# Kernel tuning notes

Measured on AMD Instinct MI355X. Metric: run time of the kernel, lower is better.

The kernel has to match this reference:

```python
import jax, jax.numpy as jnp
import numpy as np

IN_FEATURES = 1024
OUT_FEATURES = 1024
NUM_GRIDS = 8
GRID_MIN, GRID_MAX = -2.0, 2.0
DENOM = (GRID_MAX - GRID_MIN) / (NUM_GRIDS - 1)
LN_EPS = 1e-5
GRID = jnp.linspace(GRID_MIN, GRID_MAX, NUM_GRIDS)


def setup_inputs() -> dict:
    key = jax.random.key(0)
    k_x, k_sw, k_bw = jax.random.split(key, 3)
    N = 8192
    x = jax.random.normal(k_x, (N, IN_FEATURES), dtype=jnp.float32)
    ln_gamma = jnp.ones((IN_FEATURES,), dtype=jnp.float32)
    ln_beta = jnp.zeros((IN_FEATURES,), dtype=jnp.float32)
    # trunc_normal(std=0.1) approximated by scaled normal
    spline_w = 0.1 * jax.random.normal(k_sw, (OUT_FEATURES, IN_FEATURES * NUM_GRIDS), dtype=jnp.float32)
    base_w = jax.random.normal(k_bw, (OUT_FEATURES, IN_FEATURES), dtype=jnp.float32) * (1.0 / np.sqrt(IN_FEATURES))
    base_b = jnp.zeros((OUT_FEATURES,), dtype=jnp.float32)
    return {"x": x, "ln_gamma": ln_gamma, "ln_beta": ln_beta,
            "spline_w": spline_w, "base_w": base_w, "base_b": base_b}


def reference(x, ln_gamma, ln_beta, spline_w, base_w, base_b):
    # LayerNorm over last dim
    mu = jnp.mean(x, axis=-1, keepdims=True)
    var = jnp.var(x, axis=-1, keepdims=True)
    xn = (x - mu) * jax.lax.rsqrt(var + LN_EPS) * ln_gamma + ln_beta
    # RBF basis: [N, in, G]
    basis = jnp.exp(-jnp.square((xn[..., None] - GRID) / DENOM))
    basis = basis.reshape(x.shape[0], IN_FEATURES * NUM_GRIDS)
    y = jnp.einsum('nk,ok->no', basis, spline_w)
    y = y + jnp.einsum('nd,od->no', jax.nn.silu(x), base_w) + base_b
    return y
```

## Files before the change

kernel.cpp:

```cpp
#include <hip/hip_runtime.h>
#include <hip/hip_bf16.h>
#include <stdint.h>

#define IN_F 1024
#define OUT_F 1024
#define NG 8
#define KSPLINE 8192
#define KDIM 9216
#define M_ROWS 8192
#define LOG2E 1.4426950408889634f
#define DENOMV 0.5714285714285714f
#define INV_DENOM 1.75f

using bf16_t = __bf16;
using bf16x8 = __attribute__((ext_vector_type(8))) __bf16;
using f32x4  = __attribute__((ext_vector_type(4))) float;

#define AS1 __attribute__((address_space(1)))
#define AS3 __attribute__((address_space(3)))

__device__ inline unsigned short f2bf(float f) {
    unsigned int u = __float_as_uint(f);
    u += 0x7fffu + ((u >> 16) & 1u);
    return (unsigned short)(u >> 16);
}

__global__ __launch_bounds__(256) void prep_w_kernel(
        const float* __restrict__ sw, const float* __restrict__ bw,
        bf16_t* __restrict__ W) {
    int idx = blockIdx.x * 256 + threadIdx.x;
    int o   = idx / 2304;
    int k4  = idx - o * 2304;
    float4 v;
    if (k4 < 2048) v = ((const float4*)sw)[(size_t)o * 2048 + k4];
    else           v = ((const float4*)bw)[(size_t)o * 256 + (k4 - 2048)];
    unsigned int lo = (unsigned int)f2bf(v.x) | ((unsigned int)f2bf(v.y) << 16);
    unsigned int hi = (unsigned int)f2bf(v.z) | ((unsigned int)f2bf(v.w) << 16);
    ((uint2*)W)[idx] = make_uint2(lo, hi);
}

__global__ __launch_bounds__(256) void prep_a_kernel(
        const float* __restrict__ x, const float* __restrict__ gamma,
        const float* __restrict__ beta, bf16_t* __restrict__ A) {
    int row = blockIdx.x;
    int tid = threadIdx.x;
    const float4 xv = ((const float4*)(x + (size_t)row * IN_F))[tid];
    float s  = xv.x + xv.y + xv.z + xv.w;
    float s2 = xv.x * xv.x + xv.y * xv.y + xv.z * xv.z + xv.w * xv.w;
#pragma unroll
    for (int off = 32; off > 0; off >>= 1) {
        s  += __shfl_down(s, off);
        s2 += __shfl_down(s2, off);
    }
    __shared__ float red[8];
    int wave = tid >> 6, lane = tid & 63;
    if (lane == 0) { red[wave] = s; red[4 + wave] = s2; }
    __syncthreads();
    s  = red[0] + red[1] + red[2] + red[3];
    s2 = red[4] + red[5] + red[6] + red[7];
    float mu   = s * (1.0f / IN_F);
    float var  = s2 * (1.0f / IN_F) - mu * mu;
    float rstd = rsqrtf(var + 1e-5f);

    bf16_t* Arow = A + (size_t)row * KDIM;
    float xa[4] = {xv.x, xv.y, xv.z, xv.w};
    unsigned short silu_us[4];
#pragma unroll
    for (int j = 0; j < 4; ++j) {
        int f = tid * 4 + j;
        float xs = xa[j];
        float xn = (xs - mu) * rstd * gamma[f] + beta[f];
        unsigned int pk[4];
#pragma unroll
        for (int g = 0; g < 4; ++g) {
            float t0 = (xn - (-2.0f + (float)(2 * g)     * DENOMV)) * INV_DENOM;
            float t1 = (xn - (-2.0f + (float)(2 * g + 1) * DENOMV)) * INV_DENOM;
            float b0 = exp2f(t0 * t0 * -LOG2E);
            float b1 = exp2f(t1 * t1 * -LOG2E);
            pk[g] = (unsigned int)f2bf(b0) | ((unsigned int)f2bf(b1) << 16);
        }
        ((uint4*)(Arow + (size_t)f * NG))[0] = make_uint4(pk[0], pk[1], pk[2], pk[3]);
        float sg = xs / (1.0f + exp2f(-xs * LOG2E));
        silu_us[j] = f2bf(sg);
    }
    unsigned int slo = (unsigned int)silu_us[0] | ((unsigned int)silu_us[1] << 16);
    unsigned int shi = (unsigned int)silu_us[2] | ((unsigned int)silu_us[3] << 16);
    ((uint2*)(Arow + KSPLINE))[tid] = make_uint2(slo, shi);
}

__global__ __launch_bounds__(256, 2) void gemm_kernel(
        const bf16_t* __restrict__ A, const bf16_t* __restrict__ W,
        const float* __restrict__ bias, float* __restrict__ C) {
    __shared__ alignas(16) bf16_t As[128 * 32];
    __shared__ alignas(16) bf16_t Bs[128 * 32];
    const int bm = blockIdx.x, bn = blockIdx.y;
    const int tid = threadIdx.x;
    const int wave = tid >> 6, lane = tid & 63;
    const int wm = wave >> 1, wn = wave & 1;

    f32x4 acc[4][4] = {};

    const bf16_t* gAj[2];
    const bf16_t* gBj[2];
    int ldsOff[2];
#pragma unroll
    for (int j = 0; j < 2; ++j) {
        int chunk = wave * 128 + j * 64 + lane;
        int r  = chunk >> 2;
        int c8 = (chunk & 3) * 8;
        gAj[j] = A + (size_t)(bm * 128 + r) * KDIM + c8;
        gBj[j] = W + (size_t)(bn * 128 + r) * KDIM + c8;
        ldsOff[j] = chunk * 8;
    }

    const int lm = lane & 15;
    const int lk = (lane >> 4) * 8;

    for (int kt = 0; kt < KDIM / 32; ++kt) {
        __syncthreads();
#pragma unroll
        for (int j = 0; j < 2; ++j) {
            __builtin_amdgcn_global_load_lds(
                (const AS1 void*)(gAj[j] + kt * 32), (AS3 void*)(As + ldsOff[j]), 16, 0, 0);
            __builtin_amdgcn_global_load_lds(
                (const AS1 void*)(gBj[j] + kt * 32), (AS3 void*)(Bs + ldsOff[j]), 16, 0, 0);
        }
        __syncthreads();

        bf16x8 a[4], b[4];
#pragma unroll
        for (int i = 0; i < 4; ++i) {
            a[i] = *(const bf16x8*)(As + (wm * 64 + i * 16 + lm) * 32 + lk);
            b[i] = *(const bf16x8*)(Bs + (wn * 64 + i * 16 + lm) * 32 + lk);
        }
#pragma unroll
        for (int mi = 0; mi < 4; ++mi)
#pragma unroll
            for (int ni = 0; ni < 4; ++ni)
                acc[mi][ni] = __builtin_amdgcn_mfma_f32_16x16x32_bf16(
                    a[mi], b[ni], acc[mi][ni], 0, 0, 0);
    }

    const int cn = lane & 15;
    const int rm = (lane >> 4) * 4;
#pragma unroll
    for (int ni = 0; ni < 4; ++ni) {
        int col = bn * 128 + wn * 64 + ni * 16 + cn;
        float bv = bias[col];
#pragma unroll
        for (int mi = 0; mi < 4; ++mi) {
            int row = bm * 128 + wm * 64 + mi * 16 + rm;
            float* Cp = C + (size_t)row * OUT_F + col;
#pragma unroll
            for (int r = 0; r < 4; ++r)
                Cp[(size_t)r * OUT_F] = acc[mi][ni][r] + bv;
        }
    }
}

extern "C" void kernel_launch(void* const* d_in, const int* in_sizes, int n_in,
                              void* d_out, int out_size, void* d_ws, size_t ws_size,
                              hipStream_t stream) {
    const float* x     = (const float*)d_in[0];
    const float* gamma = (const float*)d_in[1];
    const float* beta  = (const float*)d_in[2];
    const float* sw    = (const float*)d_in[3];
    const float* bw    = (const float*)d_in[4];
    const float* bb    = (const float*)d_in[5];
    float* out = (float*)d_out;

    char* ws = (char*)d_ws;
    const size_t Wbytes = (size_t)OUT_F * KDIM * 2;
    bf16_t* Wb = (bf16_t*)ws;
    bf16_t* Ab = (bf16_t*)(ws + Wbytes);

    const size_t rowBytes = (size_t)KDIM * 2;
    size_t avail = ws_size > Wbytes ? ws_size - Wbytes : 0;
    int chunk = (int)(avail / rowBytes);
    chunk &= ~127;
    if (chunk > M_ROWS) chunk = M_ROWS;
    if (chunk < 128) chunk = 128;

    prep_w_kernel<<<(OUT_F * 2304) / 256, 256, 0, stream>>>(sw, bw, Wb);

    for (int r0 = 0; r0 < M_ROWS; r0 += chunk) {
        int rows = (M_ROWS - r0) < chunk ? (M_ROWS - r0) : chunk;
        prep_a_kernel<<<rows, 256, 0, stream>>>(x + (size_t)r0 * IN_F, gamma, beta, Ab);
        dim3 g(rows / 128, OUT_F / 128);
        gemm_kernel<<<g, dim3(256), 0, stream>>>(Ab, Wb, bb, out + (size_t)r0 * OUT_F);
    }
}
```

Measured before the change: 346.8 us.

## Split GEMM K dimension across two blocks with atomic accumulation

```diff
diff --git a/kernel.cpp b/kernel.cpp
--- a/kernel.cpp
+++ b/kernel.cpp
@@ -8,6 +8,8 @@
 #define KSPLINE 8192
 #define KDIM 9216
 #define M_ROWS 8192
+#define SPLITK 2
+#define KHALF (KDIM / SPLITK)
 #define LOG2E 1.4426950408889634f
 #define DENOMV 0.5714285714285714f
 #define INV_DENOM 1.75f
@@ -44,9 +46,12 @@
         const float* __restrict__ beta, bf16_t* __restrict__ A) {
     int row = blockIdx.x;
     int tid = threadIdx.x;
-    const float4 xv = ((const float4*)(x + (size_t)row * IN_F))[tid];
-    float s  = xv.x + xv.y + xv.z + xv.w;
-    float s2 = xv.x * xv.x + xv.y * xv.y + xv.z * xv.z + xv.w * xv.w;
+    const float* xr = x + (size_t)row * IN_F;
+    float xv[4];
+#pragma unroll
+    for (int j = 0; j < 4; ++j) xv[j] = xr[j * 256 + tid];
+    float s  = xv[0] + xv[1] + xv[2] + xv[3];
+    float s2 = xv[0]*xv[0] + xv[1]*xv[1] + xv[2]*xv[2] + xv[3]*xv[3];
 #pragma unroll
     for (int off = 32; off > 0; off >>= 1) {
         s  += __shfl_down(s, off);
@@ -63,12 +68,12 @@
     float rstd = rsqrtf(var + 1e-5f);
 
     bf16_t* Arow = A + (size_t)row * KDIM;
-    float xa[4] = {xv.x, xv.y, xv.z, xv.w};
-    unsigned short silu_us[4];
+    uint4* basis_out = (uint4*)Arow;
+    unsigned short* silu_out = (unsigned short*)(Arow + KSPLINE);
 #pragma unroll
     for (int j = 0; j < 4; ++j) {
-        int f = tid * 4 + j;
-        float xs = xa[j];
+        int f = j * 256 + tid;
+        float xs = xv[j];
         float xn = (xs - mu) * rstd * gamma[f] + beta[f];
         unsigned int pk[4];
 #pragma unroll
@@ -79,24 +84,22 @@
             float b1 = exp2f(t1 * t1 * -LOG2E);
             pk[g] = (unsigned int)f2bf(b0) | ((unsigned int)f2bf(b1) << 16);
         }
-        ((uint4*)(Arow + (size_t)f * NG))[0] = make_uint4(pk[0], pk[1], pk[2], pk[3]);
+        basis_out[f] = make_uint4(pk[0], pk[1], pk[2], pk[3]);
         float sg = xs / (1.0f + exp2f(-xs * LOG2E));
-        silu_us[j] = f2bf(sg);
+        silu_out[f] = f2bf(sg);
     }
-    unsigned int slo = (unsigned int)silu_us[0] | ((unsigned int)silu_us[1] << 16);
-    unsigned int shi = (unsigned int)silu_us[2] | ((unsigned int)silu_us[3] << 16);
-    ((uint2*)(Arow + KSPLINE))[tid] = make_uint2(slo, shi);
 }
 
-__global__ __launch_bounds__(256, 2) void gemm_kernel(
+__global__ __launch_bounds__(256, 4) void gemm_kernel(
         const bf16_t* __restrict__ A, const bf16_t* __restrict__ W,
         const float* __restrict__ bias, float* __restrict__ C) {
     __shared__ alignas(16) bf16_t As[128 * 32];
     __shared__ alignas(16) bf16_t Bs[128 * 32];
-    const int bm = blockIdx.x, bn = blockIdx.y;
+    const int bm = blockIdx.x, bn = blockIdx.y, bz = blockIdx.z;
     const int tid = threadIdx.x;
     const int wave = tid >> 6, lane = tid & 63;
     const int wm = wave >> 1, wn = wave & 1;
+    const int k0 = bz * KHALF;
 
     f32x4 acc[4][4] = {};
 
@@ -108,15 +111,15 @@
         int chunk = wave * 128 + j * 64 + lane;
         int r  = chunk >> 2;
         int c8 = (chunk & 3) * 8;
-        gAj[j] = A + (size_t)(bm * 128 + r) * KDIM + c8;
-        gBj[j] = W + (size_t)(bn * 128 + r) * KDIM + c8;
+        gAj[j] = A + (size_t)(bm * 128 + r) * KDIM + k0 + c8;
+        gBj[j] = W + (size_t)(bn * 128 + r) * KDIM + k0 + c8;
         ldsOff[j] = chunk * 8;
     }
 
     const int lm = lane & 15;
     const int lk = (lane >> 4) * 8;
 
-    for (int kt = 0; kt < KDIM / 32; ++kt) {
+    for (int kt = 0; kt < KHALF / 32; ++kt) {
         __syncthreads();
 #pragma unroll
         for (int j = 0; j < 2; ++j) {
@@ -146,14 +149,14 @@
 #pragma unroll
     for (int ni = 0; ni < 4; ++ni) {
         int col = bn * 128 + wn * 64 + ni * 16 + cn;
-        float bv = bias[col];
+        float bv = (bz == 0) ? bias[col] : 0.0f;
 #pragma unroll
         for (int mi = 0; mi < 4; ++mi) {
             int row = bm * 128 + wm * 64 + mi * 16 + rm;
             float* Cp = C + (size_t)row * OUT_F + col;
 #pragma unroll
             for (int r = 0; r < 4; ++r)
-                Cp[(size_t)r * OUT_F] = acc[mi][ni][r] + bv;
+                atomicAdd(Cp + (size_t)r * OUT_F, acc[mi][ni][r] + bv);
         }
     }
 }
@@ -181,12 +184,14 @@
     if (chunk > M_ROWS) chunk = M_ROWS;
     if (chunk < 128) chunk = 128;
 
+    hipMemsetAsync(out, 0, (size_t)out_size * sizeof(float), stream);
+
     prep_w_kernel<<<(OUT_F * 2304) / 256, 256, 0, stream>>>(sw, bw, Wb);
 
     for (int r0 = 0; r0 < M_ROWS; r0 += chunk) {
         int rows = (M_ROWS - r0) < chunk ? (M_ROWS - r0) : chunk;
         prep_a_kernel<<<rows, 256, 0, stream>>>(x + (size_t)r0 * IN_F, gamma, beta, Ab);
-        dim3 g(rows / 128, OUT_F / 128);
+        dim3 g(rows / 128, OUT_F / 128, SPLITK);
         gemm_kernel<<<g, dim3(256), 0, stream>>>(Ab, Wb, bb, out + (size_t)r0 * OUT_F);
     }
 }
```

Result: no change. 345.2 us (-0.5%).
